# Kernel tuning notes

Measured on AMD Instinct MI355X. Metric: run time of the kernel, lower is better.

## Reference

```python
import jax, jax.numpy as jnp
import numpy as np

D_MODEL = 1024
NHEAD = 16
HEAD_DIM = D_MODEL // NHEAD
DIM_FF = 4096
B, TC, TP = 4, 1024, 1024
EPS = 1e-5


def _layernorm(x, g, b):
    mu = jnp.mean(x, axis=-1, keepdims=True)
    var = jnp.mean(jnp.square(x - mu), axis=-1, keepdims=True)
    return (x - mu) * jax.lax.rsqrt(var + EPS) * g + b


def setup_inputs() -> dict:
    key = jax.random.key(0)
    ks = jax.random.split(key, 12)
    s = 0.02
    return {
        "x": jax.random.normal(ks[0], (B, TC, D_MODEL), jnp.float32),
        "Kp": jax.random.normal(ks[1], (B, NHEAD, TP, HEAD_DIM), jnp.float32),
        "Vp": jax.random.normal(ks[2], (B, NHEAD, TP, HEAD_DIM), jnp.float32),
        "pos_offset": TP,
        "wqkv": jax.random.normal(ks[3], (D_MODEL, 3 * D_MODEL), jnp.float32) * s,
        "bqkv": jnp.zeros((3 * D_MODEL,), jnp.float32),
        "wo": jax.random.normal(ks[4], (D_MODEL, D_MODEL), jnp.float32) * s,
        "bo": jnp.zeros((D_MODEL,), jnp.float32),
        "g1": jnp.ones((D_MODEL,), jnp.float32),
        "be1": jnp.zeros((D_MODEL,), jnp.float32),
        "g2": jnp.ones((D_MODEL,), jnp.float32),
        "be2": jnp.zeros((D_MODEL,), jnp.float32),
        "w1": jax.random.normal(ks[5], (D_MODEL, DIM_FF), jnp.float32) * s,
        "bf1": jnp.zeros((DIM_FF,), jnp.float32),
        "w2": jax.random.normal(ks[6], (DIM_FF, D_MODEL), jnp.float32) * s,
        "bf2": jnp.zeros((D_MODEL,), jnp.float32),
    }


def reference(x, Kp, Vp, pos_offset, wqkv, bqkv, wo, bo, g1, be1, g2, be2, w1, bf1, w2, bf2):
    Bsz, Tc, D = x.shape
    H, Dh = NHEAD, HEAD_DIM
    h = _layernorm(x, g1, be1)
    qkv = (h @ wqkv + bqkv).reshape(Bsz, Tc, 3, H, Dh).transpose(2, 0, 3, 1, 4)
    q, k_new, v_new = qkv[0], qkv[1], qkv[2]  # [B,H,Tc,Dh]
    K = jnp.concatenate([Kp, k_new], axis=2)  # [B,H,Tk,Dh]
    V = jnp.concatenate([Vp, v_new], axis=2)
    Tk = K.shape[2]
    scale = Dh ** -0.5
    # fused causal-masked attention; equivalent to the per-token loop:
    # query i attends keys j with j <= pos_offset + i
    scores = jnp.einsum("bhqd,bhkd->bhqk", q, K) * scale
    q_idx = jnp.arange(Tc)[:, None]
    k_idx = jnp.arange(Tk)[None, :]
    mask = k_idx <= (pos_offset + q_idx)  # [Tc,Tk]
    scores = jnp.where(mask, scores, jnp.finfo(scores.dtype).min)
    attn = jax.nn.softmax(scores, axis=-1)
    o = jnp.einsum("bhqk,bhkd->bhqd", attn, V)
    o = o.transpose(0, 2, 1, 3).reshape(Bsz, Tc, D)
    x = x + o @ wo + bo
    h2 = _layernorm(x, g2, be2)
    ff = jax.nn.gelu(h2 @ w1 + bf1, approximate=False) @ w2 + bf2
    x = x + ff
    return x, K, V
```

## Files before the change

kernel.cpp:

```cpp
#include <hip/hip_runtime.h>
#include <math.h>

#define DM   1024
#define NH   16
#define DH   64
#define DFF  4096
#define BSZ  4
#define TCC  1024
#define TPP  1024
#define TKK  2048
#define NTOK (BSZ*TCC)

typedef __attribute__((ext_vector_type(8))) short bf16x8;
typedef __attribute__((ext_vector_type(4))) float f32x4;

__device__ __forceinline__ unsigned short f2bf(float x) {
  union { float f; unsigned u; } v; v.f = x;
  unsigned r = v.u + 0x7fffu + ((v.u >> 16) & 1u);
  return (unsigned short)(r >> 16);
}
__device__ __forceinline__ unsigned pk2(float a, float b) {
  return (unsigned)f2bf(a) | ((unsigned)f2bf(b) << 16);
}

__device__ __forceinline__ void gload16(const void* g, void* l) {
  __builtin_amdgcn_global_load_lds(
      (const __attribute__((address_space(1))) void*)g,
      (__attribute__((address_space(3))) void*)l, 16, 0, 0);
}

__device__ __forceinline__ float wave_reduce_sum(float v) {
#pragma unroll
  for (int off = 32; off > 0; off >>= 1)
    v += __shfl_down(v, off, 64);
  return v;
}

__device__ __forceinline__ float gelu_f(float x) {
  float z = fabsf(x) * 0.70710678118654752440f;
  float t = 1.0f / (1.0f + 0.3275911f * z);
  float y = t * (0.254829592f +
            t * (-0.284496736f +
            t * (1.421413741f +
            t * (-1.453152027f +
            t * 1.061405429f))));
  float e = __expf(-z * z);
  float erfz = 1.0f - y * e;
  float s = (x >= 0.0f) ? erfz : -erfz;
  return 0.5f * x * (1.0f + s);
}

__global__ __launch_bounds__(256) void castT_kernel(
    const float* __restrict__ W, unsigned short* __restrict__ Wt, int K, int N) {
  __shared__ float tile[32][33];
  int nb = blockIdx.x << 5, kb = blockIdx.y << 5;
  int c = threadIdx.x & 31, r8 = threadIdx.x >> 5;
#pragma unroll
  for (int i = 0; i < 32; i += 8)
    tile[r8 + i][c] = W[(size_t)(kb + r8 + i) * N + nb + c];
  __syncthreads();
#pragma unroll
  for (int i = 0; i < 32; i += 8)
    Wt[(size_t)(nb + r8 + i) * K + kb + c] = f2bf(tile[c][r8 + i]);
}

__global__ __launch_bounds__(256) void castVt_kernel(
    const float* __restrict__ V, unsigned short* __restrict__ Vt) {
  __shared__ float tile[32][33];
  int z = blockIdx.z;
  const float* W = V + (size_t)z * TKK * DH;
  unsigned short* Wt = Vt + (size_t)z * DH * TKK;
  int nb = blockIdx.x << 5;
  int kb = blockIdx.y << 5;
  int c = threadIdx.x & 31, r8 = threadIdx.x >> 5;
#pragma unroll
  for (int i = 0; i < 32; i += 8)
    tile[r8 + i][c] = W[(size_t)(kb + r8 + i) * DH + nb + c];
  __syncthreads();
#pragma unroll
  for (int i = 0; i < 32; i += 8)
    Wt[(size_t)(nb + r8 + i) * TKK + kb + c] = f2bf(tile[c][r8 + i]);
}

__global__ __launch_bounds__(256) void copy_kv_kernel(
    const float4* __restrict__ Kp, const float4* __restrict__ Vp,
    float4* __restrict__ Kout, float4* __restrict__ Vout,
    unsigned short* __restrict__ Kbf) {
  int idx = blockIdx.x * 256 + threadIdx.x;
  int r = idx >> 4;
  int c = idx & 15;
  int dr = (r >> 10) * TKK + (r & 1023);
  float4 kv = Kp[idx];
  Kout[dr * 16 + c] = kv;
  Vout[dr * 16 + c] = Vp[idx];
  if (Kbf != nullptr) {
    uint2 pk;
    pk.x = pk2(kv.x, kv.y);
    pk.y = pk2(kv.z, kv.w);
    *(uint2*)(Kbf + (size_t)(dr * 16 + c) * 4) = pk;
  }
}

__global__ __launch_bounds__(256) void ln_kernel(
    const float* __restrict__ x, const float* __restrict__ g,
    const float* __restrict__ b, unsigned short* __restrict__ out) {
  __shared__ float red[8];
  int row = blockIdx.x;
  int tid = threadIdx.x;
  const float4* xr = (const float4*)(x + (size_t)row * DM);
  float4 xv = xr[tid];
  float s  = xv.x + xv.y + xv.z + xv.w;
  float ss = xv.x*xv.x + xv.y*xv.y + xv.z*xv.z + xv.w*xv.w;
  s  = wave_reduce_sum(s);
  ss = wave_reduce_sum(ss);
  int lane = tid & 63, wid = tid >> 6;
  if (lane == 0) { red[wid] = s; red[4 + wid] = ss; }
  __syncthreads();
  s  = red[0] + red[1] + red[2] + red[3];
  ss = red[4] + red[5] + red[6] + red[7];
  float mu  = s * (1.0f / DM);
  float var = ss * (1.0f / DM) - mu * mu;
  float rs  = rsqrtf(var + 1e-5f);
  float4 gv = ((const float4*)g)[tid];
  float4 bv = ((const float4*)b)[tid];
  ushort4 ov;
  ov.x = f2bf((xv.x - mu) * rs * gv.x + bv.x);
  ov.y = f2bf((xv.y - mu) * rs * gv.y + bv.y);
  ov.z = f2bf((xv.z - mu) * rs * gv.z + bv.z);
  ov.w = f2bf((xv.w - mu) * rs * gv.w + bv.w);
  *(ushort4*)&out[(size_t)row * DM + tid * 4] = ov;
}

template <int MODE, int DEPTH>
__global__ __launch_bounds__(256) void mm_kernel(
    const unsigned short* __restrict__ A, const unsigned short* __restrict__ Bt,
    const float* __restrict__ bias, const float* __restrict__ res,
    float* __restrict__ outf, unsigned short* __restrict__ outb,
    float* __restrict__ Kc, float* __restrict__ Vc,
    unsigned short* __restrict__ Kbfp,
    int M, int N, int K) {
  __shared__ __align__(16) short As[DEPTH * 128 * 32];
  __shared__ __align__(16) short Bs[DEPTH * 128 * 32];
  int tid = threadIdx.x;
  int w = tid >> 6, l = tid & 63;
  int m0 = blockIdx.y << 7, n0 = blockIdx.x << 7;
  int wm = (w >> 1) << 6, wn = (w & 1) << 6;
  int cidx = l & 15, rg = l >> 4;
  f32x4 acc[4][4] = {};

  int idx0 = w * 1024 + l * 16;
  int idx1 = idx0 + 4096;
  const char* gA0 = (const char*)A + (size_t)(m0 + (idx0 >> 6)) * 2 * K + (idx0 & 63);
  const char* gA1 = (const char*)A + (size_t)(m0 + (idx1 >> 6)) * 2 * K + (idx1 & 63);
  const char* gB0 = (const char*)Bt + (size_t)(n0 + (idx0 >> 6)) * 2 * K + (idx0 & 63);
  const char* gB1 = (const char*)Bt + (size_t)(n0 + (idx1 >> 6)) * 2 * K + (idx1 & 63);

  auto stage = [&](int bsel) {
    char* base_a = (char*)As + bsel * 8192;
    char* base_b = (char*)Bs + bsel * 8192;
    gload16(gA0, base_a + idx0); gload16(gA1, base_a + idx1);
    gload16(gB0, base_b + idx0); gload16(gB1, base_b + idx1);
    gA0 += 64; gA1 += 64; gB0 += 64; gB1 += 64;
  };
  auto compute = [&](int bsel) {
    const short* pa = As + bsel * 4096;
    const short* pb = Bs + bsel * 4096;
    bf16x8 af[4], bfr[4];
#pragma unroll
    for (int i = 0; i < 4; ++i) {
      af[i]  = *(const bf16x8*)&pa[(wm + i * 16 + cidx) * 32 + rg * 8];
      bfr[i] = *(const bf16x8*)&pb[(wn + i * 16 + cidx) * 32 + rg * 8];
    }
#pragma unroll
    for (int i = 0; i < 4; ++i)
#pragma unroll
      for (int j = 0; j < 4; ++j)
        acc[i][j] = __builtin_amdgcn_mfma_f32_16x16x32_bf16(
            af[i], bfr[j], acc[i][j], 0, 0, 0);
  };

  int nt = K >> 5;
  if (DEPTH == 2) {
    stage(0);
    for (int t = 0; t < nt - 1; ++t) {
      __syncthreads();
      stage((t + 1) & 1);
      compute(t & 1);
    }
    __syncthreads();
    compute((nt - 1) & 1);
  } else {
    stage(0); stage(1); stage(2);
    for (int t = 0; t < nt - 3; ++t) {
      asm volatile("s_waitcnt vmcnt(8)" ::: "memory");
      __builtin_amdgcn_sched_barrier(0);
      __builtin_amdgcn_s_barrier();
      __builtin_amdgcn_sched_barrier(0);
      stage((t + 3) & 3);
      compute(t & 3);
    }
    asm volatile("s_waitcnt vmcnt(8)" ::: "memory");
    __builtin_amdgcn_sched_barrier(0);
    __builtin_amdgcn_s_barrier();
    __builtin_amdgcn_sched_barrier(0);
    compute((nt - 3) & 3);
    asm volatile("s_waitcnt vmcnt(4)" ::: "memory");
    __builtin_amdgcn_sched_barrier(0);
    __builtin_amdgcn_s_barrier();
    __builtin_amdgcn_sched_barrier(0);
    compute((nt - 2) & 3);
    asm volatile("s_waitcnt vmcnt(0)" ::: "memory");
    __builtin_amdgcn_sched_barrier(0);
    __builtin_amdgcn_s_barrier();
    __builtin_amdgcn_sched_barrier(0);
    compute((nt - 1) & 3);
  }

#pragma unroll
  for (int i = 0; i < 4; ++i) {
#pragma unroll
    for (int j = 0; j < 4; ++j) {
      int col = n0 + wn + j * 16 + cidx;
      float bb = bias[col];
#pragma unroll
      for (int r = 0; r < 4; ++r) {
        int row = m0 + wm + i * 16 + rg * 4 + r;
        float v = acc[i][j][r] + bb;
        if (MODE == 0) {
          int which = col >> 10, c = col & 1023;
          int hh = c >> 6, dd = c & 63;
          int b = row >> 10, t = row & 1023;
          size_t base = (size_t)(b * NH + hh);
          if (which == 0)      outb[(base * TCC + t) * DH + dd] = f2bf(v * 0.125f);
          else if (which == 1) {
            size_t off = (base * TKK + TPP + t) * DH + dd;
            Kc[off] = v;
            if (Kbfp != nullptr) Kbfp[off] = f2bf(v);
          } else               Vc[(base * TKK + TPP + t) * DH + dd] = v;
        } else if (MODE == 1) {
          size_t off = (size_t)row * N + col;
          outf[off] = res[off] + v;
        } else {
          outb[(size_t)row * N + col] = f2bf(gelu_f(v));
        }
      }
    }
  }
}

template <int KBF>
__global__ __launch_bounds__(256) void attn_kernel(
    const unsigned short* __restrict__ Qb, const float* __restrict__ K,
    const unsigned short* __restrict__ Kb16,
    const unsigned short* __restrict__ Vtb, const int* __restrict__ posp,
    unsigned short* __restrict__ o) {
  __shared__ __align__(16) unsigned short Qs[64][72];
  __shared__ __align__(16) unsigned short Ks[64][72];
  __shared__ __align__(16) unsigned short Vts[64][72];
  __shared__ __align__(16) unsigned short Pw[4][16][72];
  int tid = threadIdx.x;
  int w = tid >> 6, lane = tid & 63;
  int l15 = lane & 15, quad = lane >> 4;
  int blk = blockIdx.x;
  int bh = blk >> 4;
  int qbase = (blk & 15) << 6;
  int b = bh >> 4, h = bh & 15;
  int pos = *posp;

  {
    int r = tid >> 2, cg = (tid & 3) << 4;
    const unsigned short* src = Qb + ((size_t)bh * TCC + qbase + r) * DH + cg;
    *(uint4*)&Qs[r][cg]     = *(const uint4*)src;
    *(uint4*)&Qs[r][cg + 8] = *(const uint4*)(src + 8);
  }
  __syncthreads();
  bf16x8 aq0 = *(const bf16x8*)&Qs[16 * w + l15][quad * 8];
  bf16x8 aq1 = *(const bf16x8*)&Qs[16 * w + l15][32 + quad * 8];

  f32x4 accO[4] = {};
  f32x4 accL = {};
  bf16x8 ones;
#pragma unroll
  for (int i = 0; i < 8; ++i) ones[i] = (short)0x3F80;

  int nk = pos + qbase + 64; if (nk > TKK) nk = TKK;
  int ntiles = nk >> 6;
  const float* Kbh = K + (size_t)bh * TKK * DH;
  const unsigned short* Kbh16 = Kb16 + (size_t)bh * TKK * DH;
  const unsigned short* Vbh = Vtb + (size_t)bh * DH * TKK;

  for (int t = 0; t < ntiles; ++t) {
    int kt = t << 6;
    {
      int r = tid >> 2, cg = (tid & 3) << 4;
      if (KBF) {
        const unsigned short* ks = Kbh16 + (size_t)(kt + r) * DH + cg;
        *(uint4*)&Ks[r][cg]     = *(const uint4*)ks;
        *(uint4*)&Ks[r][cg + 8] = *(const uint4*)(ks + 8);
      } else {
        const float* ks = Kbh + (size_t)(kt + r) * DH + cg;
        float4 k0 = *(const float4*)ks,       k1 = *(const float4*)(ks + 4);
        float4 k2 = *(const float4*)(ks + 8), k3 = *(const float4*)(ks + 12);
        uint4 p0, p1;
        p0.x = pk2(k0.x, k0.y); p0.y = pk2(k0.z, k0.w);
        p0.z = pk2(k1.x, k1.y); p0.w = pk2(k1.z, k1.w);
        p1.x = pk2(k2.x, k2.y); p1.y = pk2(k2.z, k2.w);
        p1.z = pk2(k3.x, k3.y); p1.w = pk2(k3.z, k3.w);
        *(uint4*)&Ks[r][cg]     = p0;
        *(uint4*)&Ks[r][cg + 8] = p1;
      }
      const unsigned short* vs = Vbh + (size_t)r * TKK + kt + cg;
      *(uint4*)&Vts[r][cg]     = *(const uint4*)vs;
      *(uint4*)&Vts[r][cg + 8] = *(const uint4*)(vs + 8);
    }
    __syncthreads();
    f32x4 accS[4] = {};
    __builtin_amdgcn_s_setprio(1);
#pragma unroll
    for (int j = 0; j < 4; ++j) {
      bf16x8 bk0 = *(const bf16x8*)&Ks[16 * j + l15][quad * 8];
      bf16x8 bk1 = *(const bf16x8*)&Ks[16 * j + l15][32 + quad * 8];
      accS[j] = __builtin_amdgcn_mfma_f32_16x16x32_bf16(aq0, bk0, accS[j], 0, 0, 0);
      accS[j] = __builtin_amdgcn_mfma_f32_16x16x32_bf16(aq1, bk1, accS[j], 0, 0, 0);
    }
    __builtin_amdgcn_s_setprio(0);
    bool edge = (kt + 63 > pos + qbase);
#pragma unroll
    for (int j = 0; j < 4; ++j) {
      int key = kt + 16 * j + l15;
#pragma unroll
      for (int r = 0; r < 4; ++r) {
        float p = __expf(accS[j][r]);
        if (edge && key > pos + qbase + 16 * w + quad * 4 + r) p = 0.f;
        Pw[w][quad * 4 + r][16 * j + l15] = f2bf(p);
      }
    }
    bf16x8 ap0 = *(const bf16x8*)&Pw[w][l15][quad * 8];
    bf16x8 ap1 = *(const bf16x8*)&Pw[w][l15][32 + quad * 8];
    __builtin_amdgcn_s_setprio(1);
    accL = __builtin_amdgcn_mfma_f32_16x16x32_bf16(ap0, ones, accL, 0, 0, 0);
    accL = __builtin_amdgcn_mfma_f32_16x16x32_bf16(ap1, ones, accL, 0, 0, 0);
#pragma unroll
    for (int j2 = 0; j2 < 4; ++j2) {
      bf16x8 bv0 = *(const bf16x8*)&Vts[16 * j2 + l15][quad * 8];
      bf16x8 bv1 = *(const bf16x8*)&Vts[16 * j2 + l15][32 + quad * 8];
      accO[j2] = __builtin_amdgcn_mfma_f32_16x16x32_bf16(ap0, bv0, accO[j2], 0, 0, 0);
      accO[j2] = __builtin_amdgcn_mfma_f32_16x16x32_bf16(ap1, bv1, accO[j2], 0, 0, 0);
    }
    __builtin_amdgcn_s_setprio(0);
    __syncthreads();
  }
#pragma unroll
  for (int r = 0; r < 4; ++r) {
    float inv = 1.0f / accL[r];
    int qg = qbase + 16 * w + quad * 4 + r;
    size_t base = (((size_t)(b * TCC + qg)) * NH + h) * DH;
#pragma unroll
    for (int j2 = 0; j2 < 4; ++j2)
      o[base + 16 * j2 + l15] = f2bf(accO[j2][r] * inv);
  }
}

extern "C" void kernel_launch(void* const* d_in, const int* in_sizes, int n_in,
                              void* d_out, int out_size, void* d_ws, size_t ws_size,
                              hipStream_t stream) {
  (void)in_sizes; (void)n_in; (void)out_size;
  const float* x    = (const float*)d_in[0];
  const float* Kp   = (const float*)d_in[1];
  const float* Vp   = (const float*)d_in[2];
  const int*   posp = (const int*)d_in[3];
  const float* wqkv = (const float*)d_in[4];
  const float* bqkv = (const float*)d_in[5];
  const float* wo   = (const float*)d_in[6];
  const float* bo   = (const float*)d_in[7];
  const float* g1   = (const float*)d_in[8];
  const float* be1  = (const float*)d_in[9];
  const float* g2   = (const float*)d_in[10];
  const float* be2  = (const float*)d_in[11];
  const float* w1   = (const float*)d_in[12];
  const float* bf1  = (const float*)d_in[13];
  const float* w2   = (const float*)d_in[14];
  const float* bf2  = (const float*)d_in[15];

  float* xout = (float*)d_out;
  float* Kout = xout + (size_t)BSZ * TCC * DM;
  float* Vout = Kout + (size_t)BSZ * NH * TKK * DH;

  const size_t MB = 1024 * 1024;
  char* ws = (char*)d_ws;
  unsigned short* wqkvT = (unsigned short*)(ws);
  unsigned short* woT   = (unsigned short*)(ws + 6 * MB);
  unsigned short* w1T   = (unsigned short*)(ws + 8 * MB);
  unsigned short* w2T   = (unsigned short*)(ws + 16 * MB);
  unsigned short* hbf   = (unsigned short*)(ws + 24 * MB);
  unsigned short* ffbf  = (unsigned short*)(ws + 32 * MB);
  unsigned short* Qbuf  = (unsigned short*)(ws + 32 * MB);
  unsigned short* obf   = (unsigned short*)(ws + 40 * MB);
  unsigned short* Vtb   = (unsigned short*)(ws + 48 * MB);
  float*          x2    = xout;
  unsigned short* Kbf   = (ws_size >= 80 * MB)
                            ? (unsigned short*)(ws + 64 * MB) : nullptr;

  castT_kernel<<<dim3(96, 32),  dim3(256), 0, stream>>>(wqkv, wqkvT, DM, 3 * DM);
  castT_kernel<<<dim3(32, 32),  dim3(256), 0, stream>>>(wo,   woT,   DM, DM);
  castT_kernel<<<dim3(128, 32), dim3(256), 0, stream>>>(w1,   w1T,   DM, DFF);
  castT_kernel<<<dim3(32, 128), dim3(256), 0, stream>>>(w2,   w2T,   DFF, DM);

  copy_kv_kernel<<<dim3(4096), dim3(256), 0, stream>>>(
      (const float4*)Kp, (const float4*)Vp, (float4*)Kout, (float4*)Vout, Kbf);
  ln_kernel<<<dim3(NTOK), dim3(256), 0, stream>>>(x, g1, be1, hbf);
  mm_kernel<0, 2><<<dim3(24, 32), dim3(256), 0, stream>>>(
      hbf, wqkvT, bqkv, nullptr, nullptr, Qbuf, Kout, Vout, Kbf, NTOK, 3 * DM, DM);
  castVt_kernel<<<dim3(2, 64, 64), dim3(256), 0, stream>>>(Vout, Vtb);
  if (Kbf != nullptr)
    attn_kernel<1><<<dim3(1024), dim3(256), 0, stream>>>(Qbuf, Kout, Kbf, Vtb, posp, obf);
  else
    attn_kernel<0><<<dim3(1024), dim3(256), 0, stream>>>(Qbuf, Kout, Kbf, Vtb, posp, obf);
  mm_kernel<1, 4><<<dim3(8, 32), dim3(256), 0, stream>>>(
      obf, woT, bo, x, x2, nullptr, nullptr, nullptr, nullptr, NTOK, DM, DM);
  ln_kernel<<<dim3(NTOK), dim3(256), 0, stream>>>(x2, g2, be2, hbf);
  mm_kernel<2, 2><<<dim3(32, 32), dim3(256), 0, stream>>>(
      hbf, w1T, bf1, nullptr, nullptr, ffbf, nullptr, nullptr, nullptr, NTOK, DFF, DM);
  mm_kernel<1, 4><<<dim3(8, 32), dim3(256), 0, stream>>>(
      ffbf, w2T, bf2, x2, xout, nullptr, nullptr, nullptr, nullptr, NTOK, DM, DFF);
}
```

Baseline: 500.1 us.

## Add 256x256-tile 8-wave GEMM with 4-stage LDS pipeline for QKV and FF1

Introduces an mm8_kernel using 512 threads and 256x256 output tiles, a swizzled LDS layout, a 4-deep async global-to-LDS pipeline split into two halves, and setprio around MFMA bursts. It replaces the QKV projection and first FFN GEMM, aiming for more operand reuse per loaded byte and better overlap of loads with MFMA work. The old mm_kernel loses its MODE 0 path. Larger tiles give fewer blocks (192 and 256 on a 256-CU part), so occupancy and tail behaviour may suffer, and LDS use is 128KB per block.

```diff
diff --git a/kernel.cpp b/kernel.cpp
--- a/kernel.cpp
+++ b/kernel.cpp
@@ -131,13 +131,133 @@
   *(ushort4*)&out[(size_t)row * DM + tid * 4] = ov;
 }
 
+template <int MODE>
+__global__ __launch_bounds__(512) void mm8_kernel(
+    const unsigned short* __restrict__ A, const unsigned short* __restrict__ Bt,
+    const float* __restrict__ bias,
+    float* __restrict__ outf, unsigned short* __restrict__ outb,
+    float* __restrict__ Kc, float* __restrict__ Vc,
+    unsigned short* __restrict__ Kbfp,
+    int M, int N, int K) {
+  __shared__ __align__(16) short lds[4][2][8192];
+  int tid = threadIdx.x;
+  int l = tid & 63, w = tid >> 6;
+  int wr = w >> 2, wc = w & 3;
+  int cidx = l & 15, rg = l >> 4;
+  int m0 = blockIdx.y << 8, n0 = blockIdx.x << 8;
+
+  int r0 = tid >> 2;
+  int cb = (((tid & 3) ^ ((r0 >> 1) & 3)) << 4);
+  const char* gA = (const char*)A + (size_t)(m0 + r0) * 2 * K + cb;
+  const char* gB = (const char*)Bt + (size_t)(n0 + r0) * 2 * K + cb;
+  size_t rskip = (size_t)128 * 2 * K;
+
+  int xcs = ((rg ^ ((cidx >> 1) & 3)) << 4);
+  int offA = (wr * 128 + cidx) * 64 + xcs;
+  int offB = (wc * 64 + cidx) * 64 + xcs;
+
+  f32x4 acc[8][4] = {};
+  int NT = K >> 5;
+
+  auto stage = [&](int t, int half) {
+    char* la = (char*)&lds[t & 3][0][0] + tid * 16 + half * 8192;
+    char* lb = (char*)&lds[t & 3][1][0] + tid * 16 + half * 8192;
+    const char* sa = gA + t * 64 + (half ? rskip : 0);
+    const char* sb = gB + t * 64 + (half ? rskip : 0);
+    gload16(sa, la);
+    gload16(sb, lb);
+  };
+
+  stage(0, 0); stage(0, 1);
+  stage(1, 0); stage(1, 1);
+  stage(2, 0); stage(2, 1);
+  asm volatile("s_waitcnt vmcnt(8)" ::: "memory");
+  __builtin_amdgcn_sched_barrier(0);
+  __builtin_amdgcn_s_barrier();
+
+  for (int t = 0; t < NT; ++t) {
+    const char* pa = (const char*)&lds[t & 3][0][0];
+    const char* pb = (const char*)&lds[t & 3][1][0];
+    bf16x8 af[4], bg[4], a2[4];
+#pragma unroll
+    for (int i = 0; i < 4; ++i)
+      af[i] = *(const bf16x8*)(pa + offA + i * 1024);
+#pragma unroll
+    for (int j = 0; j < 4; ++j)
+      bg[j] = *(const bf16x8*)(pb + offB + j * 1024);
+    if (t + 3 < NT) stage(t + 3, 0);
+    __builtin_amdgcn_s_barrier();
+    asm volatile("s_waitcnt lgkmcnt(0)" ::: "memory");
+    __builtin_amdgcn_sched_barrier(0);
+    __builtin_amdgcn_s_setprio(1);
+#pragma unroll
+    for (int i = 0; i < 4; ++i)
+#pragma unroll
+      for (int j = 0; j < 4; ++j)
+        acc[i][j] = __builtin_amdgcn_mfma_f32_16x16x32_bf16(
+            af[i], bg[j], acc[i][j], 0, 0, 0);
+    __builtin_amdgcn_s_setprio(0);
+    __builtin_amdgcn_s_barrier();
+#pragma unroll
+    for (int i = 0; i < 4; ++i)
+      a2[i] = *(const bf16x8*)(pa + offA + (i + 4) * 1024);
+    if (t + 3 < NT) stage(t + 3, 1);
+    if (t + 3 < NT) {
+      asm volatile("s_waitcnt vmcnt(8)" ::: "memory");
+    } else if (t + 2 < NT) {
+      asm volatile("s_waitcnt vmcnt(4)" ::: "memory");
+    } else {
+      asm volatile("s_waitcnt vmcnt(0)" ::: "memory");
+    }
+    __builtin_amdgcn_sched_barrier(0);
+    __builtin_amdgcn_s_barrier();
+    asm volatile("s_waitcnt lgkmcnt(0)" ::: "memory");
+    __builtin_amdgcn_sched_barrier(0);
+    __builtin_amdgcn_s_setprio(1);
+#pragma unroll
+    for (int i = 0; i < 4; ++i)
+#pragma unroll
+      for (int j = 0; j < 4; ++j)
+        acc[i + 4][j] = __builtin_amdgcn_mfma_f32_16x16x32_bf16(
+            a2[i], bg[j], acc[i + 4][j], 0, 0, 0);
+    __builtin_amdgcn_s_setprio(0);
+    __builtin_amdgcn_s_barrier();
+  }
+
+#pragma unroll
+  for (int i = 0; i < 8; ++i) {
+#pragma unroll
+    for (int j = 0; j < 4; ++j) {
+      int col = n0 + wc * 64 + j * 16 + cidx;
+      float bb = bias[col];
+#pragma unroll
+      for (int r = 0; r < 4; ++r) {
+        int row = m0 + wr * 128 + i * 16 + rg * 4 + r;
+        float v = acc[i][j][r] + bb;
+        if (MODE == 0) {
+          int which = col >> 10, c = col & 1023;
+          int hh = c >> 6, dd = c & 63;
+          int b = row >> 10, tt = row & 1023;
+          size_t base = (size_t)(b * NH + hh);
+          if (which == 0)      outb[(base * TCC + tt) * DH + dd] = f2bf(v * 0.125f);
+          else if (which == 1) {
+            size_t off = (base * TKK + TPP + tt) * DH + dd;
+            Kc[off] = v;
+            if (Kbfp != nullptr) Kbfp[off] = f2bf(v);
+          } else               Vc[(base * TKK + TPP + tt) * DH + dd] = v;
+        } else {
+          outb[(size_t)row * N + col] = f2bf(gelu_f(v));
+        }
+      }
+    }
+  }
+}
+
 template <int MODE, int DEPTH>
 __global__ __launch_bounds__(256) void mm_kernel(
     const unsigned short* __restrict__ A, const unsigned short* __restrict__ Bt,
     const float* __restrict__ bias, const float* __restrict__ res,
     float* __restrict__ outf, unsigned short* __restrict__ outb,
-    float* __restrict__ Kc, float* __restrict__ Vc,
-    unsigned short* __restrict__ Kbfp,
     int M, int N, int K) {
   __shared__ __align__(16) short As[DEPTH * 128 * 32];
   __shared__ __align__(16) short Bs[DEPTH * 128 * 32];
@@ -226,18 +346,7 @@
       for (int r = 0; r < 4; ++r) {
         int row = m0 + wm + i * 16 + rg * 4 + r;
         float v = acc[i][j][r] + bb;
-        if (MODE == 0) {
-          int which = col >> 10, c = col & 1023;
-          int hh = c >> 6, dd = c & 63;
-          int b = row >> 10, t = row & 1023;
-          size_t base = (size_t)(b * NH + hh);
-          if (which == 0)      outb[(base * TCC + t) * DH + dd] = f2bf(v * 0.125f);
-          else if (which == 1) {
-            size_t off = (base * TKK + TPP + t) * DH + dd;
-            Kc[off] = v;
-            if (Kbfp != nullptr) Kbfp[off] = f2bf(v);
-          } else               Vc[(base * TKK + TPP + t) * DH + dd] = v;
-        } else if (MODE == 1) {
+        if (MODE == 1) {
           size_t off = (size_t)row * N + col;
           outf[off] = res[off] + v;
         } else {
@@ -409,18 +518,18 @@
   copy_kv_kernel<<<dim3(4096), dim3(256), 0, stream>>>(
       (const float4*)Kp, (const float4*)Vp, (float4*)Kout, (float4*)Vout, Kbf);
   ln_kernel<<<dim3(NTOK), dim3(256), 0, stream>>>(x, g1, be1, hbf);
-  mm_kernel<0, 2><<<dim3(24, 32), dim3(256), 0, stream>>>(
-      hbf, wqkvT, bqkv, nullptr, nullptr, Qbuf, Kout, Vout, Kbf, NTOK, 3 * DM, DM);
+  mm8_kernel<0><<<dim3(12, 16), dim3(512), 0, stream>>>(
+      hbf, wqkvT, bqkv, nullptr, Qbuf, Kout, Vout, Kbf, NTOK, 3 * DM, DM);
   castVt_kernel<<<dim3(2, 64, 64), dim3(256), 0, stream>>>(Vout, Vtb);
   if (Kbf != nullptr)
     attn_kernel<1><<<dim3(1024), dim3(256), 0, stream>>>(Qbuf, Kout, Kbf, Vtb, posp, obf);
   else
     attn_kernel<0><<<dim3(1024), dim3(256), 0, stream>>>(Qbuf, Kout, Kbf, Vtb, posp, obf);
   mm_kernel<1, 4><<<dim3(8, 32), dim3(256), 0, stream>>>(
-      obf, woT, bo, x, x2, nullptr, nullptr, nullptr, nullptr, NTOK, DM, DM);
+      obf, woT, bo, x, x2, nullptr, NTOK, DM, DM);
   ln_kernel<<<dim3(NTOK), dim3(256), 0, stream>>>(x2, g2, be2, hbf);
-  mm_kernel<2, 2><<<dim3(32, 32), dim3(256), 0, stream>>>(
-      hbf, w1T, bf1, nullptr, nullptr, ffbf, nullptr, nullptr, nullptr, NTOK, DFF, DM);
+  mm8_kernel<2><<<dim3(16, 16), dim3(512), 0, stream>>>(
+      hbf, w1T, bf1, nullptr, ffbf, nullptr, nullptr, nullptr, NTOK, DFF, DM);
   mm_kernel<1, 4><<<dim3(8, 32), dim3(256), 0, stream>>>(
-      ffbf, w2T, bf2, x2, xout, nullptr, nullptr, nullptr, nullptr, NTOK, DM, DFF);
-}
+      ffbf, w2T, bf2, x2, xout, nullptr, NTOK, DM, DFF);
+}
```

Measured after the change: 483.5 us. -3.3%, faster.
